# Kernel tuning notes

Hardware: AMD Instinct MI355X
Metric: run time of the kernel (lower is better)

Reference implementation:

```python
import jax, jax.numpy as jnp
import numpy as np

B, P, K, D, T = 512, 64, 8, 512, 50000


def setup_inputs() -> dict:
    key = jax.random.key(0)
    k1, k2, k3, k4, k5, k6 = jax.random.split(key, 6)
    return {
        "inputs": jax.random.normal(k1, (B, P, D), dtype=jnp.float32),
        "title_emb_mat": jax.random.normal(k2, (T, D), dtype=jnp.float32),
        "nbr_batch": jax.random.randint(k3, (B, P, K), 0, B, dtype=jnp.int32),
        "nbr_job": jax.random.randint(k4, (B, P, K), 0, P, dtype=jnp.int32),
        "nbr_title": jax.random.randint(k5, (B, P, K), 0, T, dtype=jnp.int32),
        "nbr_mask": jax.random.randint(k6, (B, P, K), 0, 2, dtype=jnp.int32),
    }


def reference(inputs, title_emb_mat, nbr_batch, nbr_job, nbr_title, nbr_mask):
    # inputs:        [B, P, D]  job embeddings per employee position
    # title_emb_mat: [T, Dt]    title embedding table (Dt == D here)
    # nbr_*:         [B, P, K]  padded metapath neighbor indices + validity mask
    mask = nbr_mask.astype(bool)                              # [B,P,K]
    ref_embs = inputs[nbr_batch, nbr_job]                     # [B,P,K,D] gather of neighbor job embs
    # attention logits: focal emb vs neighbor embs (raw inner product, exp-normalized)
    raw_s = jnp.einsum('bpd,bpkd->bpk', inputs, ref_embs)     # [B,P,K]
    logits = jnp.where(mask, raw_s, jnp.float32(-1e9))
    sim = jax.nn.softmax(logits, axis=-1) * mask              # exact zeros on padded slots;
    # an all-masked (i,pos) -> uniform softmax * 0 mask == 0 row (matches torch 'continue' -> zeros)
    ref_t_embs = title_emb_mat[nbr_title]                     # [B,P,K,Dt] gather of target-title embs
    graph_concat = jnp.einsum('bpk,bpkt->bpt', sim, ref_t_embs)  # [B,P,Dt]
    out = jnp.concatenate([inputs, graph_concat], axis=-1)    # [B,P,D+Dt]
    return out.reshape(B * P, D + title_emb_mat.shape[1])     # torch.cat over batch, axis=0
```

## Files before the change

### kernel.cpp

```cpp
#include <hip/hip_runtime.h>

#define BB 512
#define PP 64
#define KK 8
#define DD 512

typedef float v4f __attribute__((ext_vector_type(4)));

__global__ __launch_bounds__(256) void han_meta_kernel(
    const float* __restrict__ inputs,
    const float* __restrict__ title,
    const int*   __restrict__ nbr_batch,
    const int*   __restrict__ nbr_job,
    const int*   __restrict__ nbr_title,
    const int*   __restrict__ nbr_mask,
    float*       __restrict__ out)
{
    const int lane = threadIdx.x & 63;
    const int wave = threadIdx.x >> 6;
    const int row  = blockIdx.x * 4 + wave;

    const float4* inp4 = (const float4*)(inputs + (size_t)row * DD);
    const float4 fa = inp4[lane];
    const float4 fb = inp4[lane + 64];

    const int4* nb4 = (const int4*)(nbr_batch + row * KK);
    const int4* nj4 = (const int4*)(nbr_job   + row * KK);
    const int4* nt4 = (const int4*)(nbr_title + row * KK);
    const int4* nm4 = (const int4*)(nbr_mask  + row * KK);
    int nbk[KK], njk[KK], ntk[KK], nmk[KK];
    *(int4*)&nbk[0] = nb4[0]; *(int4*)&nbk[4] = nb4[1];
    *(int4*)&njk[0] = nj4[0]; *(int4*)&njk[4] = nj4[1];
    *(int4*)&ntk[0] = nt4[0]; *(int4*)&ntk[4] = nt4[1];
    *(int4*)&nmk[0] = nm4[0]; *(int4*)&nmk[4] = nm4[1];

    float logit[KK];
    #pragma unroll
    for (int k = 0; k < KK; ++k) {
        if (nmk[k]) {
            const float4* g4 = (const float4*)(inputs +
                ((size_t)nbk[k] * PP + (size_t)njk[k]) * DD);
            const float4 ga = g4[lane];
            const float4 gb = g4[lane + 64];
            float d = fa.x*ga.x + fa.y*ga.y + fa.z*ga.z + fa.w*ga.w
                    + fb.x*gb.x + fb.y*gb.y + fb.z*gb.z + fb.w*gb.w;
            #pragma unroll
            for (int off = 32; off >= 1; off >>= 1)
                d += __shfl_xor(d, off, 64);
            logit[k] = d;
        } else {
            logit[k] = -1e9f;
        }
    }

    float m = logit[0];
    #pragma unroll
    for (int k = 1; k < KK; ++k) m = fmaxf(m, logit[k]);
    float e[KK];
    float s = 0.0f;
    #pragma unroll
    for (int k = 0; k < KK; ++k) {
        e[k] = expf(logit[k] - m);
        s += e[k];
    }
    const float inv = 1.0f / s;

    float4 oa = make_float4(0.f, 0.f, 0.f, 0.f);
    float4 ob = make_float4(0.f, 0.f, 0.f, 0.f);
    #pragma unroll
    for (int k = 0; k < KK; ++k) {
        if (nmk[k]) {
            const float w = e[k] * inv;
            const float4* t4 = (const float4*)(title + (size_t)ntk[k] * DD);
            const float4 ta = t4[lane];
            const float4 tb = t4[lane + 64];
            oa.x += w * ta.x; oa.y += w * ta.y; oa.z += w * ta.z; oa.w += w * ta.w;
            ob.x += w * tb.x; ob.y += w * tb.y; ob.z += w * tb.z; ob.w += w * tb.w;
        }
    }

    v4f* o4 = (v4f*)(out + (size_t)row * (2 * DD));
    v4f va = {fa.x, fa.y, fa.z, fa.w};
    v4f vb = {fb.x, fb.y, fb.z, fb.w};
    v4f vc = {oa.x, oa.y, oa.z, oa.w};
    v4f vd = {ob.x, ob.y, ob.z, ob.w};
    __builtin_nontemporal_store(va, o4 + lane);
    __builtin_nontemporal_store(vb, o4 + lane + 64);
    __builtin_nontemporal_store(vc, o4 + lane + 128);
    __builtin_nontemporal_store(vd, o4 + lane + 192);
}

extern "C" void kernel_launch(void* const* d_in, const int* in_sizes, int n_in,
                              void* d_out, int out_size, void* d_ws, size_t ws_size,
                              hipStream_t stream) {
    const float* inputs    = (const float*)d_in[0];
    const float* title     = (const float*)d_in[1];
    const int*   nbr_batch = (const int*)d_in[2];
    const int*   nbr_job   = (const int*)d_in[3];
    const int*   nbr_title = (const int*)d_in[4];
    const int*   nbr_mask  = (const int*)d_in[5];
    float*       out       = (float*)d_out;

    const int rows = BB * PP;
    dim3 grid(rows / 4);
    dim3 block(256);
    han_meta_kernel<<<grid, block, 0, stream>>>(
        inputs, title, nbr_batch, nbr_job, nbr_title, nbr_mask, out);
}
```

Before: 296.5 us.

## Split into attention and title-aggregation kernels with batched gather loads

Splits the single kernel into two passes. The first computes softmax weights, writes them to workspace, and stores the input half of the output. The second gathers title rows using those weights and writes the aggregated half. Each pass now issues all eight neighbor gathers before computing, and the eight shuffle reductions are interleaved, to raise memory-level parallelism. Splitting also separates the inputs working set from the large title table, which may improve cache behavior. The costs are an extra launch, a workspace round-trip, and higher register pressure from holding eight float4 pairs at once.

Result: slower. 302.8 us (+2.1%).

```diff
diff --git a/kernel.cpp b/kernel.cpp
--- a/kernel.cpp
+++ b/kernel.cpp
@@ -7,14 +7,14 @@
 
 typedef float v4f __attribute__((ext_vector_type(4)));
 
-__global__ __launch_bounds__(256) void han_meta_kernel(
+
+__global__ __launch_bounds__(256) void han_pass1(
     const float* __restrict__ inputs,
-    const float* __restrict__ title,
     const int*   __restrict__ nbr_batch,
     const int*   __restrict__ nbr_job,
-    const int*   __restrict__ nbr_title,
     const int*   __restrict__ nbr_mask,
-    float*       __restrict__ out)
+    float*       __restrict__ out,
+    float*       __restrict__ sim_ws)
 {
     const int lane = threadIdx.x & 63;
     const int wave = threadIdx.x >> 6;
@@ -26,66 +26,112 @@
 
     const int4* nb4 = (const int4*)(nbr_batch + row * KK);
     const int4* nj4 = (const int4*)(nbr_job   + row * KK);
-    const int4* nt4 = (const int4*)(nbr_title + row * KK);
     const int4* nm4 = (const int4*)(nbr_mask  + row * KK);
-    int nbk[KK], njk[KK], ntk[KK], nmk[KK];
+    int nbk[KK], njk[KK], nmk[KK];
     *(int4*)&nbk[0] = nb4[0]; *(int4*)&nbk[4] = nb4[1];
     *(int4*)&njk[0] = nj4[0]; *(int4*)&njk[4] = nj4[1];
-    *(int4*)&ntk[0] = nt4[0]; *(int4*)&ntk[4] = nt4[1];
     *(int4*)&nmk[0] = nm4[0]; *(int4*)&nmk[4] = nm4[1];
 
-    float logit[KK];
+    float4 ga[KK], gb[KK];
     #pragma unroll
     for (int k = 0; k < KK; ++k) {
         if (nmk[k]) {
             const float4* g4 = (const float4*)(inputs +
                 ((size_t)nbk[k] * PP + (size_t)njk[k]) * DD);
-            const float4 ga = g4[lane];
-            const float4 gb = g4[lane + 64];
-            float d = fa.x*ga.x + fa.y*ga.y + fa.z*ga.z + fa.w*ga.w
-                    + fb.x*gb.x + fb.y*gb.y + fb.z*gb.z + fb.w*gb.w;
-            #pragma unroll
-            for (int off = 32; off >= 1; off >>= 1)
-                d += __shfl_xor(d, off, 64);
-            logit[k] = d;
+            ga[k] = g4[lane];
+            gb[k] = g4[lane + 64];
         } else {
-            logit[k] = -1e9f;
+            ga[k] = make_float4(0.f,0.f,0.f,0.f);
+            gb[k] = make_float4(0.f,0.f,0.f,0.f);
         }
     }
 
+    float d[KK];
+    #pragma unroll
+    for (int k = 0; k < KK; ++k) {
+        d[k] = fa.x*ga[k].x + fa.y*ga[k].y + fa.z*ga[k].z + fa.w*ga[k].w
+             + fb.x*gb[k].x + fb.y*gb[k].y + fb.z*gb[k].z + fb.w*gb[k].w;
+    }
+
+    #pragma unroll
+    for (int off = 32; off >= 1; off >>= 1) {
+        #pragma unroll
+        for (int k = 0; k < KK; ++k)
+            d[k] += __shfl_xor(d[k], off, 64);
+    }
+
+    float logit[KK];
+    #pragma unroll
+    for (int k = 0; k < KK; ++k) logit[k] = nmk[k] ? d[k] : -1e9f;
     float m = logit[0];
     #pragma unroll
     for (int k = 1; k < KK; ++k) m = fmaxf(m, logit[k]);
-    float e[KK];
-    float s = 0.0f;
+    float e[KK]; float s = 0.0f;
     #pragma unroll
-    for (int k = 0; k < KK; ++k) {
-        e[k] = expf(logit[k] - m);
-        s += e[k];
-    }
+    for (int k = 0; k < KK; ++k) { e[k] = expf(logit[k] - m); s += e[k]; }
     const float inv = 1.0f / s;
 
-    float4 oa = make_float4(0.f, 0.f, 0.f, 0.f);
-    float4 ob = make_float4(0.f, 0.f, 0.f, 0.f);
+    float sim[KK];
     #pragma unroll
-    for (int k = 0; k < KK; ++k) {
-        if (nmk[k]) {
-            const float w = e[k] * inv;
-            const float4* t4 = (const float4*)(title + (size_t)ntk[k] * DD);
-            const float4 ta = t4[lane];
-            const float4 tb = t4[lane + 64];
-            oa.x += w * ta.x; oa.y += w * ta.y; oa.z += w * ta.z; oa.w += w * ta.w;
-            ob.x += w * tb.x; ob.y += w * tb.y; ob.z += w * tb.z; ob.w += w * tb.w;
-        }
+    for (int k = 0; k < KK; ++k) sim[k] = nmk[k] ? e[k] * inv : 0.0f;
+
+    if (lane < 2) {
+        float4 sv = lane == 0 ? make_float4(sim[0],sim[1],sim[2],sim[3])
+                              : make_float4(sim[4],sim[5],sim[6],sim[7]);
+        ((float4*)(sim_ws + (size_t)row * KK))[lane] = sv;
     }
 
     v4f* o4 = (v4f*)(out + (size_t)row * (2 * DD));
     v4f va = {fa.x, fa.y, fa.z, fa.w};
     v4f vb = {fb.x, fb.y, fb.z, fb.w};
+    __builtin_nontemporal_store(va, o4 + lane);
+    __builtin_nontemporal_store(vb, o4 + lane + 64);
+}
+
+__global__ __launch_bounds__(256) void han_pass2(
+    const float* __restrict__ title,
+    const int*   __restrict__ nbr_title,
+    const float* __restrict__ sim_ws,
+    float*       __restrict__ out)
+{
+    const int lane = threadIdx.x & 63;
+    const int wave = threadIdx.x >> 6;
+    const int row  = blockIdx.x * 4 + wave;
+
+    const int4* nt4 = (const int4*)(nbr_title + row * KK);
+    int ntk[KK];
+    *(int4*)&ntk[0] = nt4[0]; *(int4*)&ntk[4] = nt4[1];
+
+    const float4* s4 = (const float4*)(sim_ws + (size_t)row * KK);
+    float sim[KK];
+    *(float4*)&sim[0] = s4[0]; *(float4*)&sim[4] = s4[1];
+
+    float4 ta[KK], tb[KK];
+    #pragma unroll
+    for (int k = 0; k < KK; ++k) {
+        if (sim[k] != 0.0f) {
+            const float4* t4 = (const float4*)(title + (size_t)ntk[k] * DD);
+            ta[k] = t4[lane];
+            tb[k] = t4[lane + 64];
+        }
+    }
+
+    float4 oa = make_float4(0.f,0.f,0.f,0.f);
+    float4 ob = make_float4(0.f,0.f,0.f,0.f);
+    #pragma unroll
+    for (int k = 0; k < KK; ++k) {
+        if (sim[k] != 0.0f) {
+            const float w = sim[k];
+            oa.x += w * ta[k].x; oa.y += w * ta[k].y;
+            oa.z += w * ta[k].z; oa.w += w * ta[k].w;
+            ob.x += w * tb[k].x; ob.y += w * tb[k].y;
+            ob.z += w * tb[k].z; ob.w += w * tb[k].w;
+        }
+    }
+
+    v4f* o4 = (v4f*)(out + (size_t)row * (2 * DD));
     v4f vc = {oa.x, oa.y, oa.z, oa.w};
     v4f vd = {ob.x, ob.y, ob.z, ob.w};
-    __builtin_nontemporal_store(va, o4 + lane);
-    __builtin_nontemporal_store(vb, o4 + lane + 64);
     __builtin_nontemporal_store(vc, o4 + lane + 128);
     __builtin_nontemporal_store(vd, o4 + lane + 192);
 }
@@ -100,10 +146,13 @@
     const int*   nbr_title = (const int*)d_in[4];
     const int*   nbr_mask  = (const int*)d_in[5];
     float*       out       = (float*)d_out;
+    float*       sim_ws    = (float*)d_ws;
 
     const int rows = BB * PP;
     dim3 grid(rows / 4);
     dim3 block(256);
-    han_meta_kernel<<<grid, block, 0, stream>>>(
-        inputs, title, nbr_batch, nbr_job, nbr_title, nbr_mask, out);
+    han_pass1<<<grid, block, 0, stream>>>(
+        inputs, nbr_batch, nbr_job, nbr_mask, out, sim_ws);
+    han_pass2<<<grid, block, 0, stream>>>(
+        title, nbr_title, sim_ws, out);
 }
```
